# Kernel tuning notes

Measured on AMD Instinct MI355X. Metric: run time of the kernel, lower is better.

## Reference

```python
import jax, jax.numpy as jnp
import numpy as np

B, S, H, DH = 8, 2048, 4, 32
D = H * DH  # all_head_size = true_hidden_size = 128


def setup_inputs() -> dict:
    key = jax.random.key(0)
    ks = jax.random.split(key, 9)
    inp = {
        "query_tensor": jax.random.normal(ks[0], (B, S, D), dtype=jnp.float32),
        "key_tensor": jax.random.normal(ks[1], (B, S, D), dtype=jnp.float32),
        "value_tensor": jax.random.normal(ks[2], (B, S, D), dtype=jnp.float32),
        "attention_mask": jnp.zeros((B, 1, 1, S), dtype=jnp.float32),
        "head_mask": jnp.ones((1, H, 1, 1), dtype=jnp.float32),
        "Wq": jax.random.normal(ks[3], (D, D), dtype=jnp.float32) * 0.02,
        "bq": jnp.zeros((D,), dtype=jnp.float32),
        "Wk": jax.random.normal(ks[4], (D, D), dtype=jnp.float32) * 0.02,
        "bk": jnp.zeros((D,), dtype=jnp.float32),
        "Wv": jax.random.normal(ks[5], (D, D), dtype=jnp.float32) * 0.02,
        "bv": jnp.zeros((D,), dtype=jnp.float32),
    }
    return inp


def _split_heads(x):
    # (B, S, D) -> (B, H, S, DH)
    return x.reshape(B, S, H, DH).transpose(0, 2, 1, 3)


def reference(query_tensor, key_tensor, value_tensor, attention_mask, head_mask,
              Wq, bq, Wk, bk, Wv, bv):
    q = _split_heads(query_tensor @ Wq + bq)   # (B,H,S,DH)
    k = _split_heads(key_tensor @ Wk + bk)
    v = _split_heads(value_tensor @ Wv + bv)

    scale = 1.0 / jnp.sqrt(jnp.float32(DH))
    scores = jnp.einsum("bhqd,bhkd->bhqk", q, k) * scale + attention_mask
    probs = jax.nn.softmax(scores, axis=-1)
    # dropout is identity at inference (training=False)
    probs = probs * head_mask
    ctx = jnp.einsum("bhqk,bhkd->bhqd", probs, v)  # (B,H,S,DH)
    ctx = ctx.transpose(0, 2, 1, 3).reshape(B, S, D)
    return ctx
```

## Files before the change

kernel.cpp:

```cpp
#include <hip/hip_runtime.h>
#include <hip/hip_bf16.h>
#include <math.h>

#define B_ 8
#define S_ 2048
#define H_ 4
#define DH_ 32
#define D_ 128
#define BS_ (B_ * S_)
#define NT_ 32
#define LOG2E 1.4426950408889634f
#define QSCALE (0.17677669529663687f * LOG2E)

typedef float f32x4 __attribute__((ext_vector_type(4)));
typedef short s16x8 __attribute__((ext_vector_type(8)));

__device__ __forceinline__ unsigned short bf(float x) {
    return __builtin_bit_cast(unsigned short, __float2bfloat16(x));
}
__device__ __forceinline__ float bf2f(unsigned short u) {
    return __builtin_bit_cast(float, (unsigned int)u << 16);
}
__device__ __forceinline__ unsigned int pk2(float a, float b) {
    return (unsigned int)bf(a) | ((unsigned int)bf(b) << 16);
}
__device__ __forceinline__ void gll16(const void* g, void* l) {
    __builtin_amdgcn_global_load_lds(
        (const __attribute__((address_space(1))) unsigned int*)(g),
        (__attribute__((address_space(3))) unsigned int*)(l), 16, 0, 0);
}

__global__ __launch_bounds__(256) void wprep(
    const float* __restrict__ Wq, const float* __restrict__ Wk, const float* __restrict__ Wv,
    const float* __restrict__ maskg,
    unsigned short* __restrict__ Wt, unsigned short* __restrict__ Em)
{
    if (blockIdx.z == 3) {
        const int id16 = blockIdx.y * 4 + blockIdx.x;
        const int base = id16 * 1024 + threadIdx.x * 4;
        float4 m4 = *(const float4*)&maskg[base];
        ushort4 o;
        o.x = bf(__builtin_amdgcn_exp2f(m4.x * LOG2E));
        o.y = bf(__builtin_amdgcn_exp2f(m4.y * LOG2E));
        o.z = bf(__builtin_amdgcn_exp2f(m4.z * LOG2E));
        o.w = bf(__builtin_amdgcn_exp2f(m4.w * LOG2E));
        *(ushort4*)&Em[base] = o;
        return;
    }
    const float* W = (blockIdx.z == 0) ? Wq : (blockIdx.z == 1) ? Wk : Wv;
    unsigned short* Oh = Wt + (size_t)blockIdx.z * D_ * D_;
    unsigned short* Ol = Oh + 3 * D_ * D_;
    __shared__ float tf[32][36];
    const int t = threadIdx.x;
    const int kt = blockIdx.x * 32, ct = blockIdx.y * 32;
    {
        int kl = t >> 3, cl = (t & 7) * 4;
        float4 w4 = *(const float4*)&W[(size_t)(kt + kl) * D_ + ct + cl];
        tf[kl][cl + 0] = w4.x; tf[kl][cl + 1] = w4.y;
        tf[kl][cl + 2] = w4.z; tf[kl][cl + 3] = w4.w;
    }
    __syncthreads();
    {
        int cl = t >> 3, kl = (t & 7) * 4;
        ushort4 oh, ol;
        float v;
        v = tf[kl + 0][cl]; oh.x = bf(v); ol.x = bf(v - bf2f(oh.x));
        v = tf[kl + 1][cl]; oh.y = bf(v); ol.y = bf(v - bf2f(oh.y));
        v = tf[kl + 2][cl]; oh.z = bf(v); ol.z = bf(v - bf2f(oh.z));
        v = tf[kl + 3][cl]; oh.w = bf(v); ol.w = bf(v - bf2f(oh.w));
        *(ushort4*)&Oh[(size_t)(ct + cl) * D_ + kt + kl] = oh;
        *(ushort4*)&Ol[(size_t)(ct + cl) * D_ + kt + kl] = ol;
    }
}

__global__ __launch_bounds__(256) void qkv_mfma(
    const float* __restrict__ Xq, const float* __restrict__ Xk, const float* __restrict__ Xv,
    const unsigned short* __restrict__ Wt, const float* __restrict__ maskg,
    const float* __restrict__ bq, const float* __restrict__ bk, const float* __restrict__ bv,
    unsigned short* __restrict__ Qo, unsigned short* __restrict__ Ko,
    unsigned short* __restrict__ Vt)
{
    const int mode = blockIdx.z, chalf = blockIdx.y;
    const float* X; const float* bias; unsigned short* O; float scl;
    if (mode == 0)      { X = Xq; bias = bq; O = Qo; scl = QSCALE; }
    else if (mode == 1) { X = Xk; bias = bk; O = Ko; scl = 1.f; }
    else                { X = Xv; bias = bv; O = Vt; scl = 1.f; }
    const unsigned short* WmH = Wt + (size_t)mode * D_ * D_;
    const unsigned short* WmL = WmH + 3 * D_ * D_;

    __shared__ __align__(16) unsigned short xa[2 * 32 * 136];
    __shared__ __align__(16) unsigned short wt[2 * 64 * 136];

    const int t = threadIdx.x;
    const long row0 = (long)blockIdx.x * 32;

    #pragma unroll
    for (int j = 0; j < 8; j++) {
        int idx = t + 256 * j;
        int part = idx >> 10, i2 = idx & 1023;
        int r = i2 >> 4, c16 = i2 & 15;
        const unsigned short* src = part ? WmL : WmH;
        uint4 v = *(const uint4*)&src[(size_t)(chalf * 64 + r) * D_ + c16 * 8];
        *(uint4*)&wt[part * 8704 + r * 136 + c16 * 8] = v;
    }
    #pragma unroll
    for (int j = 0; j < 4; j++) {
        int idx = t + 256 * j;
        int r = idx >> 5, c4 = idx & 31;
        float4 v = *(const float4*)(X + (row0 + r) * D_ + c4 * 4);
        ushort4 ph, pl;
        ph.x = bf(v.x); pl.x = bf(v.x - bf2f(ph.x));
        ph.y = bf(v.y); pl.y = bf(v.y - bf2f(ph.y));
        ph.z = bf(v.z); pl.z = bf(v.z - bf2f(ph.z));
        ph.w = bf(v.w); pl.w = bf(v.w - bf2f(ph.w));
        *(ushort4*)&xa[r * 136 + c4 * 4] = ph;
        *(ushort4*)&xa[4352 + r * 136 + c4 * 4] = pl;
    }
    __syncthreads();

    const int w = t >> 6, lane = t & 63, lo = lane & 15, hi = lane >> 4;
    const int mf = w >> 1, nb = (w & 1) * 2;
    f32x4 acc[2] = {};
    #pragma unroll
    for (int kk = 0; kk < 4; kk++) {
        const int ko = kk * 32 + hi * 8;
        s16x8 ah = *(const s16x8*)&xa[(mf * 16 + lo) * 136 + ko];
        s16x8 al = *(const s16x8*)&xa[4352 + (mf * 16 + lo) * 136 + ko];
        #pragma unroll
        for (int n2 = 0; n2 < 2; n2++) {
            const int nf = nb + n2;
            s16x8 bh2 = *(const s16x8*)&wt[(nf * 16 + lo) * 136 + ko];
            s16x8 bl2 = *(const s16x8*)&wt[8704 + (nf * 16 + lo) * 136 + ko];
            acc[n2] = __builtin_amdgcn_mfma_f32_16x16x32_bf16(ah, bh2, acc[n2], 0, 0, 0);
            acc[n2] = __builtin_amdgcn_mfma_f32_16x16x32_bf16(al, bh2, acc[n2], 0, 0, 0);
            acc[n2] = __builtin_amdgcn_mfma_f32_16x16x32_bf16(ah, bl2, acc[n2], 0, 0, 0);
        }
    }
    __syncthreads();

    if (mode < 2) {
        #pragma unroll
        for (int n2 = 0; n2 < 2; n2++) {
            int c_l = (nb + n2) * 16 + lo;
            float bb = bias[chalf * 64 + c_l];
            #pragma unroll
            for (int r = 0; r < 4; r++) {
                int s = mf * 16 + hi * 4 + r;
                xa[s * 72 + c_l] = bf((acc[n2][r] + bb) * scl);
            }
        }
        __syncthreads();
        int s = t >> 3, part = t & 7;
        int c_g = chalf * 64 + part * 8;
        int h = c_g >> 5, d = c_g & 31;
        long b_i = (row0 + s) >> 11, s_i = (row0 + s) & 2047;
        unsigned short* orow = O + ((b_i * H_ + h) * (long)S_ + s_i) * DH_ + d;
        *(uint4*)orow = *(const uint4*)&xa[s * 72 + part * 8];
    } else {
        const long b_i = row0 >> 11;
        const long s0g = row0 & 2047;
        float emr[4];
        #pragma unroll
        for (int r = 0; r < 4; r++) {
            const int s_l = mf * 16 + hi * 4 + r;
            emr[r] = __builtin_amdgcn_exp2f(maskg[b_i * S_ + s0g + s_l] * LOG2E);
        }
        #pragma unroll
        for (int n2 = 0; n2 < 2; n2++) {
            int c_l = (nb + n2) * 16 + lo;
            float bb = bias[chalf * 64 + c_l];
            #pragma unroll
            for (int r = 0; r < 4; r++) {
                int s = mf * 16 + hi * 4 + r;
                xa[c_l * 68 + s] = bf((acc[n2][r] + bb) * emr[r]);
            }
        }
        __syncthreads();
        if (t < 128) {
            int c_l = t >> 1, sh2 = (t & 1) * 16;
            int c_g = chalf * 64 + c_l;
            int h = c_g >> 5, d = c_g & 31;
            long s_i = s0g + sh2;
            unsigned short* orow = O + ((b_i * H_ + h) * (long)DH_ + d) * S_ + s_i;
            uint2 p0 = *(const uint2*)&xa[c_l * 68 + sh2 + 0];
            uint2 p1 = *(const uint2*)&xa[c_l * 68 + sh2 + 4];
            uint2 p2 = *(const uint2*)&xa[c_l * 68 + sh2 + 8];
            uint2 p3 = *(const uint2*)&xa[c_l * 68 + sh2 + 12];
            *(uint4*)&orow[0] = make_uint4(p0.x, p0.y, p1.x, p1.y);
            *(uint4*)&orow[8] = make_uint4(p2.x, p2.y, p3.x, p3.y);
        }
    }
}

__global__ __launch_bounds__(256) void flash_mfma(
    const unsigned short* __restrict__ Qg, const unsigned short* __restrict__ Kg,
    const unsigned short* __restrict__ Vtg, const unsigned short* __restrict__ Emg,
    const float* __restrict__ head_mask, float* __restrict__ Out)
{
    __shared__ __align__(16) unsigned short ks[2][64][32];
    __shared__ __align__(16) unsigned short vs[2][32][72];
    __shared__ __align__(16) unsigned short ps[4][32][72];

    const int t = threadIdx.x, w = t >> 6, lane = t & 63;
    const int lo = lane & 15, hi = lane >> 4;

    const int lid = blockIdx.x;
    const int swz = (lid & 7) * 64 + (lid >> 3);
    const int qi = swz & 15, bh = swz >> 4;
    const int b = bh >> 2, h = bh & 3;

    const size_t kvbase = (size_t)bh * S_ * DH_;
    const size_t vtbase = (size_t)bh * DH_ * S_;
    const unsigned short* emb = Emg + (size_t)b * S_;
    const int q0 = qi * 128 + w * 32;

    s16x8 qf[2];
    #pragma unroll
    for (int nt = 0; nt < 2; nt++)
        qf[nt] = *(const s16x8*)(Qg + kvbase + (size_t)(q0 + nt * 16 + lo) * DH_ + hi * 8);

    const float hm = head_mask[h];
    const int vd = t >> 3, vk = (t & 7) * 8;

    gll16(Kg + kvbase + (size_t)w * 16 * DH_ + (size_t)lane * 8, &ks[0][w * 16][0]);
    *(uint4*)&vs[0][vd][vk] = *(const uint4*)(Vtg + vtbase + (size_t)vd * S_ + vk);
    __syncthreads();

    f32x4 ctx[2][2] = {};
    f32x4 lacc[2] = {};
    const f32x4 z4 = {0.f, 0.f, 0.f, 0.f};
    uint4 vreg;

    for (int tile = 0; tile < NT_; tile++) {
        const int cur = tile & 1, nxt = cur ^ 1;

        if (tile < NT_ - 1) {
            gll16(Kg + kvbase + (size_t)(tile + 1) * 64 * DH_ + (size_t)w * 16 * DH_ + (size_t)lane * 8,
                  &ks[nxt][w * 16][0]);
            vreg = *(const uint4*)(Vtg + vtbase + (size_t)vd * S_ + (tile + 1) * 64 + vk);
        }
        s16x8 ef0 = *(const s16x8*)(emb + tile * 64 + hi * 8);
        s16x8 ef1 = *(const s16x8*)(emb + tile * 64 + 32 + hi * 8);

        float sv[2][16];
        __builtin_amdgcn_s_setprio(1);
        #pragma unroll
        for (int mt = 0; mt < 4; mt++) {
            s16x8 kf = *(const s16x8*)&ks[cur][mt * 16 + lo][hi * 8];
            #pragma unroll
            for (int nt = 0; nt < 2; nt++) {
                f32x4 d = __builtin_amdgcn_mfma_f32_16x16x32_bf16(kf, qf[nt], z4, 0, 0, 0);
                #pragma unroll
                for (int r = 0; r < 4; r++) sv[nt][mt * 4 + r] = d[r];
            }
        }
        __builtin_amdgcn_s_setprio(0);

        #pragma unroll
        for (int nt = 0; nt < 2; nt++) {
            #pragma unroll
            for (int mt = 0; mt < 4; mt++) {
                float p0 = __builtin_amdgcn_exp2f(sv[nt][mt * 4 + 0]);
                float p1 = __builtin_amdgcn_exp2f(sv[nt][mt * 4 + 1]);
                float p2 = __builtin_amdgcn_exp2f(sv[nt][mt * 4 + 2]);
                float p3 = __builtin_amdgcn_exp2f(sv[nt][mt * 4 + 3]);
                uint2 u = make_uint2(pk2(p0, p1), pk2(p2, p3));
                *(uint2*)&ps[w][nt * 16 + lo][mt * 16 + hi * 4] = u;
            }
        }

        __builtin_amdgcn_s_setprio(1);
        #pragma unroll
        for (int k2 = 0; k2 < 2; k2++) {
            s16x8 pa0 = *(const s16x8*)&ps[w][lo][k2 * 32 + hi * 8];
            s16x8 pa1 = *(const s16x8*)&ps[w][16 + lo][k2 * 32 + hi * 8];
            s16x8 ef = k2 ? ef1 : ef0;
            lacc[0] = __builtin_amdgcn_mfma_f32_16x16x32_bf16(pa0, ef, lacc[0], 0, 0, 0);
            lacc[1] = __builtin_amdgcn_mfma_f32_16x16x32_bf16(pa1, ef, lacc[1], 0, 0, 0);
            #pragma unroll
            for (int nd = 0; nd < 2; nd++) {
                s16x8 vb = *(const s16x8*)&vs[cur][nd * 16 + lo][k2 * 32 + hi * 8];
                ctx[0][nd] = __builtin_amdgcn_mfma_f32_16x16x32_bf16(pa0, vb, ctx[0][nd], 0, 0, 0);
                ctx[1][nd] = __builtin_amdgcn_mfma_f32_16x16x32_bf16(pa1, vb, ctx[1][nd], 0, 0, 0);
            }
        }
        __builtin_amdgcn_s_setprio(0);

        if (tile < NT_ - 1) {
            *(uint4*)&vs[nxt][vd][vk] = vreg;
            __syncthreads();
        }
    }

    #pragma unroll
    for (int mtq = 0; mtq < 2; mtq++) {
        f32x4 inv;
        #pragma unroll
        for (int r = 0; r < 4; r++) inv[r] = hm / lacc[mtq][r];
        #pragma unroll
        for (int nd = 0; nd < 2; nd++) {
            #pragma unroll
            for (int r = 0; r < 4; r++) {
                size_t sq = (size_t)q0 + mtq * 16 + hi * 4 + r;
                Out[((size_t)b * S_ + sq) * D_ + h * DH_ + nd * 16 + lo] = ctx[mtq][nd][r] * inv[r];
            }
        }
    }
}

extern "C" void kernel_launch(void* const* d_in, const int* in_sizes, int n_in,
                              void* d_out, int out_size, void* d_ws, size_t ws_size,
                              hipStream_t stream) {
    const float* Xq   = (const float*)d_in[0];
    const float* Xk   = (const float*)d_in[1];
    const float* Xv   = (const float*)d_in[2];
    const float* mask = (const float*)d_in[3];
    const float* hm   = (const float*)d_in[4];
    const float* Wq   = (const float*)d_in[5];
    const float* bq   = (const float*)d_in[6];
    const float* Wk   = (const float*)d_in[7];
    const float* bk   = (const float*)d_in[8];
    const float* Wv   = (const float*)d_in[9];
    const float* bv   = (const float*)d_in[10];
    float* out = (float*)d_out;

    unsigned short* Qo = (unsigned short*)d_ws;
    unsigned short* Ko = Qo + (size_t)2097152;
    unsigned short* Vt = Ko + (size_t)2097152;
    unsigned short* Wt = Vt + (size_t)2097152;
    unsigned short* Em = Wt + (size_t)98304;

    wprep<<<dim3(4, 4, 4), 256, 0, stream>>>(Wq, Wk, Wv, mask, Wt, Em);
    qkv_mfma<<<dim3(BS_ / 32, 2, 3), 256, 0, stream>>>(Xq, Xk, Xv, Wt, mask, bq, bk, bv, Qo, Ko, Vt);
    flash_mfma<<<dim3(512), 256, 0, stream>>>(Qo, Ko, Vt, Em, hm, out);
}
```

Baseline: 64.67 us.

## Halve queries per wave, double flash grid, swizzle K LDS layout

The attention kernel now gives each wave 16 query rows instead of 32, so the grid grows from 512 to 1024 blocks and per-thread register state (ctx, lacc, scores) shrinks. The exp2/pack step is fused into the QK MFMA loop, and the K tile is written to and read from LDS with an XOR chunk swizzle to avoid bank conflicts. The block-to-(batch,head) mapping is remapped so each XCD handles fixed heads, which helps L2 reuse of K/V. The cost is that every K/V tile is loaded from global memory twice as often in total, and each block does less MFMA work per LDS tile it loads.

```diff
diff --git a/kernel.cpp b/kernel.cpp
--- a/kernel.cpp
+++ b/kernel.cpp
@@ -199,89 +199,73 @@
 {
     __shared__ __align__(16) unsigned short ks[2][64][32];
     __shared__ __align__(16) unsigned short vs[2][32][72];
-    __shared__ __align__(16) unsigned short ps[4][32][72];
+    __shared__ __align__(16) unsigned short ps[4][16][72];
 
     const int t = threadIdx.x, w = t >> 6, lane = t & 63;
     const int lo = lane & 15, hi = lane >> 4;
 
     const int lid = blockIdx.x;
-    const int swz = (lid & 7) * 64 + (lid >> 3);
-    const int qi = swz & 15, bh = swz >> 4;
+    const int xcd = lid & 7, ser = lid >> 3;
+    const int bh = xcd + 8 * (ser >> 5);
+    const int qi = ser & 31;
     const int b = bh >> 2, h = bh & 3;
 
     const size_t kvbase = (size_t)bh * S_ * DH_;
     const size_t vtbase = (size_t)bh * DH_ * S_;
     const unsigned short* emb = Emg + (size_t)b * S_;
-    const int q0 = qi * 128 + w * 32;
-
-    s16x8 qf[2];
-    #pragma unroll
-    for (int nt = 0; nt < 2; nt++)
-        qf[nt] = *(const s16x8*)(Qg + kvbase + (size_t)(q0 + nt * 16 + lo) * DH_ + hi * 8);
+    const int q0 = qi * 64 + w * 16;
+
+    s16x8 qf = *(const s16x8*)(Qg + kvbase + (size_t)(q0 + lo) * DH_ + hi * 8);
 
     const float hm = head_mask[h];
     const int vd = t >> 3, vk = (t & 7) * 8;
-
-    gll16(Kg + kvbase + (size_t)w * 16 * DH_ + (size_t)lane * 8, &ks[0][w * 16][0]);
+    const int krow = lane >> 2, kchunk = (lane & 3) ^ (krow & 3);
+    const size_t koff = (size_t)(w * 16 + krow) * DH_ + kchunk * 8;
+
+    gll16(Kg + kvbase + koff, &ks[0][w * 16][0]);
     *(uint4*)&vs[0][vd][vk] = *(const uint4*)(Vtg + vtbase + (size_t)vd * S_ + vk);
     __syncthreads();
 
-    f32x4 ctx[2][2] = {};
-    f32x4 lacc[2] = {};
+    f32x4 ctx[2] = {};
+    f32x4 lacc = {};
     const f32x4 z4 = {0.f, 0.f, 0.f, 0.f};
     uint4 vreg;
 
+    const int kread = (hi ^ (lo & 3)) * 8;
+
     for (int tile = 0; tile < NT_; tile++) {
         const int cur = tile & 1, nxt = cur ^ 1;
 
         if (tile < NT_ - 1) {
-            gll16(Kg + kvbase + (size_t)(tile + 1) * 64 * DH_ + (size_t)w * 16 * DH_ + (size_t)lane * 8,
-                  &ks[nxt][w * 16][0]);
+            gll16(Kg + kvbase + (size_t)(tile + 1) * 64 * DH_ + koff, &ks[nxt][w * 16][0]);
             vreg = *(const uint4*)(Vtg + vtbase + (size_t)vd * S_ + (tile + 1) * 64 + vk);
         }
         s16x8 ef0 = *(const s16x8*)(emb + tile * 64 + hi * 8);
         s16x8 ef1 = *(const s16x8*)(emb + tile * 64 + 32 + hi * 8);
 
-        float sv[2][16];
         __builtin_amdgcn_s_setprio(1);
         #pragma unroll
         for (int mt = 0; mt < 4; mt++) {
-            s16x8 kf = *(const s16x8*)&ks[cur][mt * 16 + lo][hi * 8];
-            #pragma unroll
-            for (int nt = 0; nt < 2; nt++) {
-                f32x4 d = __builtin_amdgcn_mfma_f32_16x16x32_bf16(kf, qf[nt], z4, 0, 0, 0);
-                #pragma unroll
-                for (int r = 0; r < 4; r++) sv[nt][mt * 4 + r] = d[r];
-            }
+            s16x8 kf = *(const s16x8*)&ks[cur][mt * 16 + lo][kread];
+            f32x4 d = __builtin_amdgcn_mfma_f32_16x16x32_bf16(kf, qf, z4, 0, 0, 0);
+            float p0 = __builtin_amdgcn_exp2f(d[0]);
+            float p1 = __builtin_amdgcn_exp2f(d[1]);
+            float p2 = __builtin_amdgcn_exp2f(d[2]);
+            float p3 = __builtin_amdgcn_exp2f(d[3]);
+            uint2 u = make_uint2(pk2(p0, p1), pk2(p2, p3));
+            *(uint2*)&ps[w][lo][mt * 16 + hi * 4] = u;
         }
         __builtin_amdgcn_s_setprio(0);
 
-        #pragma unroll
-        for (int nt = 0; nt < 2; nt++) {
-            #pragma unroll
-            for (int mt = 0; mt < 4; mt++) {
-                float p0 = __builtin_amdgcn_exp2f(sv[nt][mt * 4 + 0]);
-                float p1 = __builtin_amdgcn_exp2f(sv[nt][mt * 4 + 1]);
-                float p2 = __builtin_amdgcn_exp2f(sv[nt][mt * 4 + 2]);
-                float p3 = __builtin_amdgcn_exp2f(sv[nt][mt * 4 + 3]);
-                uint2 u = make_uint2(pk2(p0, p1), pk2(p2, p3));
-                *(uint2*)&ps[w][nt * 16 + lo][mt * 16 + hi * 4] = u;
-            }
-        }
-
         __builtin_amdgcn_s_setprio(1);
         #pragma unroll
         for (int k2 = 0; k2 < 2; k2++) {
-            s16x8 pa0 = *(const s16x8*)&ps[w][lo][k2 * 32 + hi * 8];
-            s16x8 pa1 = *(const s16x8*)&ps[w][16 + lo][k2 * 32 + hi * 8];
-            s16x8 ef = k2 ? ef1 : ef0;
-            lacc[0] = __builtin_amdgcn_mfma_f32_16x16x32_bf16(pa0, ef, lacc[0], 0, 0, 0);
-            lacc[1] = __builtin_amdgcn_mfma_f32_16x16x32_bf16(pa1, ef, lacc[1], 0, 0, 0);
+            s16x8 pa = *(const s16x8*)&ps[w][lo][k2 * 32 + hi * 8];
+            lacc = __builtin_amdgcn_mfma_f32_16x16x32_bf16(pa, k2 ? ef1 : ef0, lacc, 0, 0, 0);
             #pragma unroll
             for (int nd = 0; nd < 2; nd++) {
                 s16x8 vb = *(const s16x8*)&vs[cur][nd * 16 + lo][k2 * 32 + hi * 8];
-                ctx[0][nd] = __builtin_amdgcn_mfma_f32_16x16x32_bf16(pa0, vb, ctx[0][nd], 0, 0, 0);
-                ctx[1][nd] = __builtin_amdgcn_mfma_f32_16x16x32_bf16(pa1, vb, ctx[1][nd], 0, 0, 0);
+                ctx[nd] = __builtin_amdgcn_mfma_f32_16x16x32_bf16(pa, vb, ctx[nd], 0, 0, 0);
             }
         }
         __builtin_amdgcn_s_setprio(0);
@@ -292,18 +276,15 @@
         }
     }
 
-    #pragma unroll
-    for (int mtq = 0; mtq < 2; mtq++) {
-        f32x4 inv;
-        #pragma unroll
-        for (int r = 0; r < 4; r++) inv[r] = hm / lacc[mtq][r];
-        #pragma unroll
-        for (int nd = 0; nd < 2; nd++) {
-            #pragma unroll
-            for (int r = 0; r < 4; r++) {
-                size_t sq = (size_t)q0 + mtq * 16 + hi * 4 + r;
-                Out[((size_t)b * S_ + sq) * D_ + h * DH_ + nd * 16 + lo] = ctx[mtq][nd][r] * inv[r];
-            }
+    f32x4 inv;
+    #pragma unroll
+    for (int r = 0; r < 4; r++) inv[r] = hm / lacc[r];
+    #pragma unroll
+    for (int nd = 0; nd < 2; nd++) {
+        #pragma unroll
+        for (int r = 0; r < 4; r++) {
+            size_t sq = (size_t)q0 + hi * 4 + r;
+            Out[((size_t)b * S_ + sq) * D_ + h * DH_ + nd * 16 + lo] = ctx[nd][r] * inv[r];
         }
     }
 }
@@ -332,5 +313,5 @@
 
     wprep<<<dim3(4, 4, 4), 256, 0, stream>>>(Wq, Wk, Wv, mask, Wt, Em);
     qkv_mfma<<<dim3(BS_ / 32, 2, 3), 256, 0, stream>>>(Xq, Xk, Xv, Wt, mask, bq, bk, bv, Qo, Ko, Vt);
-    flash_mfma<<<dim3(512), 256, 0, stream>>>(Qo, Ko, Vt, Em, hm, out);
-}
+    flash_mfma<<<dim3(1024), 256, 0, stream>>>(Qo, Ko, Vt, Em, hm, out);
+}
```

Result: faster. 62.84 us (-2.8%).
